# Performance work log

Hardware: AMD Instinct MI355X
Metric: run time of the kernel (lower is better)

Reference implementation:

```python
import jax, jax.numpy as jnp
import numpy as np

EMBED_DIM = 1024
NUM_HEADS = 16
HEAD_DIM = EMBED_DIM // NUM_HEADS
SCALE = HEAD_DIM ** -0.5


def setup_inputs() -> dict:
    key = jax.random.key(0)
    ks = jax.random.split(key, 13)
    B, Q, K, E = 2, 1024, 2048, EMBED_DIM
    bound = 1.0 / np.sqrt(E)
    def lin(k1, k2):
        W = jax.random.uniform(k1, (E, E), jnp.float32, -bound, bound)
        b = jax.random.uniform(k2, (E,), jnp.float32, -bound, bound)
        return W, b
    Wq, bq = lin(ks[0], ks[1])
    Wk, bk = lin(ks[2], ks[3])
    Wv, bv = lin(ks[4], ks[5])
    Wo, bo = lin(ks[6], ks[7])
    return {
        "query": jax.random.normal(ks[8], (B, Q, E), jnp.float32),
        "key": jax.random.normal(ks[9], (B, K, E), jnp.float32),
        "value": jax.random.normal(ks[10], (B, K, E), jnp.float32),
        "key_padding_mask": jax.random.randint(ks[11], (B, K), 0, 2).astype(bool),
        "Wq": Wq, "bq": bq, "Wk": Wk, "bk": bk,
        "Wv": Wv, "bv": bv, "Wo": Wo, "bo": bo,
    }


def reference(query, key, value, key_padding_mask, Wq, bq, Wk, bk, Wv, bv, Wo, bo):
    B, Q, E = query.shape
    K = key.shape[1]
    H, D = NUM_HEADS, HEAD_DIM
    # projections (torch Linear: x @ W.T + b)
    q = (query @ Wq.T + bq).reshape(B, Q, H, D).transpose(0, 2, 1, 3)  # [B,H,Q,D]
    k = (key @ Wk.T + bk).reshape(B, K, H, D).transpose(0, 2, 1, 3)    # [B,H,K,D]
    v = (value @ Wv.T + bv).reshape(B, K, H, D).transpose(0, 2, 1, 3)  # [B,H,K,D]
    logits = jnp.einsum('bhqd,bhkd->bhqk', q, k) * SCALE               # [B,H,Q,K]
    logits = jnp.where(key_padding_mask[:, None, None, :], -jnp.inf, logits)
    attn = jax.nn.softmax(logits, axis=-1)
    out = jnp.einsum('bhqk,bhkd->bhqd', attn, v)                        # [B,H,Q,D]
    out = out.transpose(0, 2, 1, 3).reshape(B, Q, E)
    out = out @ Wo.T + bo
    return out
```

## Files before the change

kernel.cpp:

```cpp
#include <hip/hip_runtime.h>

typedef __bf16 bf16_t;
typedef __bf16 bf16x4 __attribute__((ext_vector_type(4)));
typedef __bf16 bf16x8 __attribute__((ext_vector_type(8)));
typedef float f32x4 __attribute__((ext_vector_type(4)));

#define B_ 2
#define H_ 16
#define D_ 64
#define E_ 1024
#define QL 1024
#define KL 2048
#define SCALE_L2E 0.1803368801111204f
#define NEG_BIG -1e30f
#define DEFER_THR 8.0f

__device__ __forceinline__ void gload_lds16(const void* g, void* lds) {
  auto* gp = reinterpret_cast<const __attribute__((address_space(1))) uint32_t*>(
      reinterpret_cast<uintptr_t>(g));
  auto* lp = reinterpret_cast<__attribute__((address_space(3))) uint32_t*>(
      reinterpret_cast<uintptr_t>(lds));
  __builtin_amdgcn_global_load_lds(gp, lp, 16, 0, 0);
}

__global__ __launch_bounds__(256) void cast_all(
    const float* __restrict__ q, const float* __restrict__ k, const float* __restrict__ v,
    const float* __restrict__ wq, const float* __restrict__ wk,
    const float* __restrict__ wv, const float* __restrict__ wo,
    bf16_t* __restrict__ oq, bf16_t* __restrict__ ok, bf16_t* __restrict__ ov,
    bf16_t* __restrict__ owq, bf16_t* __restrict__ owk,
    bf16_t* __restrict__ owv, bf16_t* __restrict__ owo,
    const unsigned char* __restrict__ mraw, float* __restrict__ mbias) {
  __shared__ int flagMis, flagB0;
  int blk = blockIdx.x;
  if (blk == 7168) {
    int t = threadIdx.x;
    if (t == 0) { flagMis = 0; flagB0 = 0; }
    __syncthreads();
    int a = 0, c = 0;
    for (int i = t; i < B_ * KL; i += 256) {
      if (i & 3) a |= mraw[i]; else c |= mraw[i];
    }
    if (a) atomicOr(&flagMis, 1);
    if (c) atomicOr(&flagB0, 1);
    __syncthreads();
    int mode = (flagMis == 0) ? 0 : (flagB0 ? 1 : 2);
    for (int i = t; i < B_ * KL; i += 256) {
      int mv;
      if (mode == 0)      mv = ((const int*)mraw)[i];
      else if (mode == 1) mv = mraw[i];
      else                mv = (((const float*)mraw)[i] != 0.0f);
      mbias[i] = mv ? NEG_BIG : 0.0f;
    }
    return;
  }
  const float* in; bf16_t* out; int base;
  if (blk < 1024)      { in = q;  out = oq;  base = blk; }
  else if (blk < 3072) { in = k;  out = ok;  base = blk - 1024; }
  else if (blk < 5120) { in = v;  out = ov;  base = blk - 3072; }
  else if (blk < 5632) { in = wq; out = owq; base = blk - 5120; }
  else if (blk < 6144) { in = wk; out = owk; base = blk - 5632; }
  else if (blk < 6656) { in = wv; out = owv; base = blk - 6144; }
  else                 { in = wo; out = owo; base = blk - 6656; }
  size_t i = (size_t)base * 256 + threadIdx.x;
  float4 a = ((const float4*)in)[2 * i];
  float4 b = ((const float4*)in)[2 * i + 1];
  bf16x8 o;
  o[0] = (bf16_t)a.x; o[1] = (bf16_t)a.y; o[2] = (bf16_t)a.z; o[3] = (bf16_t)a.w;
  o[4] = (bf16_t)b.x; o[5] = (bf16_t)b.y; o[6] = (bf16_t)b.z; o[7] = (bf16_t)b.w;
  ((bf16x8*)out)[i] = o;
}

__global__ __launch_bounds__(256, 2)
void qkv_gemm(const bf16_t* __restrict__ Xq, const bf16_t* __restrict__ Xk,
              const bf16_t* __restrict__ Xv, const bf16_t* __restrict__ Wqb,
              const bf16_t* __restrict__ Wkb, const bf16_t* __restrict__ Wvb,
              const float* __restrict__ bq, const float* __restrict__ bk,
              const float* __restrict__ bv,
              bf16_t* __restrict__ qhd, bf16_t* __restrict__ khd, bf16_t* __restrict__ vht) {
  __shared__ alignas(16) bf16_t As[2][128 * 64];
  __shared__ alignas(16) bf16_t Bs[2][128 * 64];
  const int wid = blockIdx.x;
  const int work = (wid & 7) * 80 + (wid >> 3);

  const bf16_t *A, *W;
  const float* bias;
  bf16_t* out;
  int mode, Lshift, row0, col0;
  if (work < 128) {
    A = Xq; W = Wqb; bias = bq; out = qhd; mode = 0; Lshift = 10;
    row0 = (work >> 3) * 128; col0 = (work & 7) * 128;
  } else if (work < 384) {
    int t = work - 128;
    A = Xk; W = Wkb; bias = bk; out = khd; mode = 0; Lshift = 11;
    row0 = (t >> 3) * 128; col0 = (t & 7) * 128;
  } else {
    int t = work - 384;
    A = Wvb; W = Xv; bias = bv; out = vht; mode = 2; Lshift = 0;
    row0 = (t & 7) * 128; col0 = (t >> 3) * 128;
  }

  const int K = 1024;
  const int tid = threadIdx.x;
  const int lane = tid & 63;
  const int w = tid >> 6;
  const int l15 = lane & 15, l4 = lane >> 4;
  const int wr = w >> 1, wc = w & 1;

  f32x4 acc[4][4] = {};

  auto stage = [&](int buf, int kt) {
    const int k0 = kt * 64;
#pragma unroll
    for (int i = 0; i < 4; ++i) {
      int idx = (w * 4 + i) * 64 + lane;
      int r = idx >> 3, c = idx & 7;
      int cs = ((c ^ (r & 7)) * 8);
      gload_lds16(A + (size_t)(row0 + r) * K + k0 + cs, &As[buf][(w * 4 + i) * 512]);
      gload_lds16(W + (size_t)(col0 + r) * K + k0 + cs, &Bs[buf][(w * 4 + i) * 512]);
    }
  };

  auto compute = [&](int buf) {
#pragma unroll
    for (int t = 0; t < 2; ++t) {
      bf16x8 af[4], bfv[4];
#pragma unroll
      for (int i = 0; i < 4; ++i) {
        int r = wr * 64 + i * 16 + l15;
        af[i] = *(const bf16x8*)&As[buf][r * 64 + (((t * 4 + l4) ^ (r & 7)) * 8)];
      }
#pragma unroll
      for (int j = 0; j < 4; ++j) {
        int r = wc * 64 + j * 16 + l15;
        bfv[j] = *(const bf16x8*)&Bs[buf][r * 64 + (((t * 4 + l4) ^ (r & 7)) * 8)];
      }
#pragma unroll
      for (int i = 0; i < 4; ++i)
#pragma unroll
        for (int j = 0; j < 4; ++j)
          acc[i][j] = __builtin_amdgcn_mfma_f32_16x16x32_bf16(af[i], bfv[j], acc[i][j], 0, 0, 0);
    }
  };

  stage(0, 0);
  const int nk = K >> 6;
  for (int kt = 0; kt < nk; ++kt) {
    __syncthreads();
    if (kt + 1 < nk) stage((kt + 1) & 1, kt + 1);
    compute(kt & 1);
  }

#pragma unroll
  for (int i = 0; i < 4; ++i) {
    int mbase = row0 + wr * 64 + i * 16 + l4 * 4;
    f32x4 bvm = {};
    if (mode == 2) bvm = *(const f32x4*)&bias[mbase];
#pragma unroll
    for (int j = 0; j < 4; ++j) {
      int n = col0 + wc * 64 + j * 16 + l15;
      float bv = (mode == 2) ? 0.f : bias[n];
#pragma unroll
      for (int r = 0; r < 4; ++r) {
        float v = acc[i][j][r] + ((mode == 2) ? bvm[r] : bv);
        int m = mbase + r;
        if (mode == 0) {
          int bi = m >> Lshift;
          int ml = m & ((1 << Lshift) - 1);
          size_t dst = ((((size_t)bi * H_ + (n >> 6)) << Lshift) + ml) * D_ + (n & 63);
          out[dst] = (bf16_t)v;
        } else {
          int hh = m >> 6, d = m & 63;
          int bi = n >> 11, kk = n & (KL - 1);
          out[((((size_t)bi * H_ + hh) << 6) + d) * KL + kk] = (bf16_t)v;
        }
      }
    }
  }
}

template <int MODE>
__global__ __launch_bounds__(256, 2)
void gemm_nt(const bf16_t* __restrict__ A, const bf16_t* __restrict__ W,
             const float* __restrict__ bias, void* __restrict__ Cout,
             int M, int N, int K, int Lshift) {
  __shared__ alignas(16) bf16_t As[2][128 * 64];
  __shared__ alignas(16) bf16_t Bs[2][128 * 64];
  const int tid = threadIdx.x;
  const int lane = tid & 63;
  const int w = tid >> 6;
  const int l15 = lane & 15, l4 = lane >> 4;
  const int wr = w >> 1, wc = w & 1;
  const int row0 = blockIdx.x * 128, col0 = blockIdx.y * 128;

  f32x4 acc[4][4] = {};

  auto stage = [&](int buf, int kt) {
    const int k0 = kt * 64;
#pragma unroll
    for (int i = 0; i < 4; ++i) {
      int idx = (w * 4 + i) * 64 + lane;
      int r = idx >> 3, c = idx & 7;
      int cs = ((c ^ (r & 7)) * 8);
      gload_lds16(A + (size_t)(row0 + r) * K + k0 + cs, &As[buf][(w * 4 + i) * 512]);
      gload_lds16(W + (size_t)(col0 + r) * K + k0 + cs, &Bs[buf][(w * 4 + i) * 512]);
    }
  };

  auto compute = [&](int buf) {
#pragma unroll
    for (int t = 0; t < 2; ++t) {
      bf16x8 af[4], bfv[4];
#pragma unroll
      for (int i = 0; i < 4; ++i) {
        int r = wr * 64 + i * 16 + l15;
        af[i] = *(const bf16x8*)&As[buf][r * 64 + (((t * 4 + l4) ^ (r & 7)) * 8)];
      }
#pragma unroll
      for (int j = 0; j < 4; ++j) {
        int r = wc * 64 + j * 16 + l15;
        bfv[j] = *(const bf16x8*)&Bs[buf][r * 64 + (((t * 4 + l4) ^ (r & 7)) * 8)];
      }
#pragma unroll
      for (int i = 0; i < 4; ++i)
#pragma unroll
        for (int j = 0; j < 4; ++j)
          acc[i][j] = __builtin_amdgcn_mfma_f32_16x16x32_bf16(af[i], bfv[j], acc[i][j], 0, 0, 0);
    }
  };

  stage(0, 0);
  const int nk = K >> 6;
  for (int kt = 0; kt < nk; ++kt) {
    __syncthreads();
    if (kt + 1 < nk) stage((kt + 1) & 1, kt + 1);
    compute(kt & 1);
  }

#pragma unroll
  for (int i = 0; i < 4; ++i) {
    int mbase = row0 + wr * 64 + i * 16 + l4 * 4;
#pragma unroll
    for (int j = 0; j < 4; ++j) {
      int n = col0 + wc * 64 + j * 16 + l15;
      float bv = bias[n];
#pragma unroll
      for (int r = 0; r < 4; ++r) {
        float v = acc[i][j][r] + bv;
        int m = mbase + r;
        ((float*)Cout)[(size_t)m * N + n] = v;
      }
    }
  }
}

__global__ __launch_bounds__(256, 4)
void attn_fused(const bf16_t* __restrict__ qh, const bf16_t* __restrict__ kh,
                const bf16_t* __restrict__ vhT, const float* __restrict__ mbias,
                float* __restrict__ opart, float* __restrict__ marr,
                float* __restrict__ larr) {
  __shared__ alignas(16) bf16_t Ksm[2][64 * 64];
  __shared__ alignas(16) bf16_t Vt[2][64 * 64];
  __shared__ alignas(16) bf16_t Ps[4][16 * 64];

  const int wid = blockIdx.x;
  const int work = (wid & 7) * 128 + (wid >> 3);
  const int qt = work & 15;
  const int half = (work >> 4) & 1;
  const int bh = work >> 5;
  const int h = bh & 15, b = bh >> 4;

  const int tid = threadIdx.x, lane = tid & 63, w = tid >> 6;
  const int l15 = lane & 15, l4 = lane >> 4;

  const bf16_t* qbase = qh + ((size_t)bh * QL + qt * 64 + w * 16) * D_;
  bf16x8 qf[2];
#pragma unroll
  for (int t = 0; t < 2; ++t)
    qf[t] = *(const bf16x8*)(qbase + l15 * D_ + t * 32 + l4 * 8);

  float m_run = NEG_BIG, l_run = 0.f;
  f32x4 o_acc[4] = {};

  const bf16_t* kbase = kh + ((size_t)bh * KL + half * (KL / 2)) * D_;
  const bf16_t* vtb = vhT + (size_t)bh * D_ * KL + half * (KL / 2);
  const int idx0 = tid, idx1 = tid + 256;
  const int r0 = idx0 >> 3, cs0 = ((idx0 & 7) ^ (r0 & 7)) * 8;
  const int r1 = idx1 >> 3, cs1 = ((idx1 & 7) ^ (r1 & 7)) * 8;
  const bf16_t* kp0 = kbase + r0 * D_ + cs0;
  const bf16_t* kp1 = kbase + r1 * D_ + cs1;
  const bf16_t* vp0 = vtb + (size_t)r0 * KL + cs0;
  const bf16_t* vp1 = vtb + (size_t)r1 * KL + cs1;
  const float* mptr = mbias + (size_t)b * KL + half * (KL / 2) + l4 * 4;

  auto stage = [&](int bufsel) {
    gload_lds16(kp0, &Ksm[bufsel][idx0 * 8]);
    gload_lds16(kp1, &Ksm[bufsel][idx1 * 8]);
    gload_lds16(vp0, &Vt[bufsel][idx0 * 8]);
    gload_lds16(vp1, &Vt[bufsel][idx1 * 8]);
    kp0 += 64 * D_; kp1 += 64 * D_; vp0 += 64; vp1 += 64;
  };

  stage(0);
  __syncthreads();

  const int NT = KL / 2 / 64;
  for (int kt = 0; kt < NT; ++kt) {
    const int buf = kt & 1;
    if (kt + 1 < NT) stage(buf ^ 1);

    f32x4 mv[4];
#pragma unroll
    for (int ct = 0; ct < 4; ++ct)
      mv[ct] = *(const f32x4*)(mptr + ct * 16);
    mptr += 64;

    f32x4 s[4] = {};
    __builtin_amdgcn_s_setprio(1);
#pragma unroll
    for (int ct = 0; ct < 4; ++ct) {
      int krow = ct * 16 + l15;
#pragma unroll
      for (int t = 0; t < 2; ++t) {
        bf16x8 kf = *(const bf16x8*)&Ksm[buf][krow * 64 + (((t * 4 + l4) ^ (krow & 7)) * 8)];
        s[ct] = __builtin_amdgcn_mfma_f32_16x16x32_bf16(kf, qf[t], s[ct], 0, 0, 0);
      }
    }
    __builtin_amdgcn_s_setprio(0);

    float sv[4][4];
    float mt = NEG_BIG;
#pragma unroll
    for (int ct = 0; ct < 4; ++ct)
#pragma unroll
      for (int r = 0; r < 4; ++r) {
        float x = s[ct][r] * SCALE_L2E + mv[ct][r];
        sv[ct][r] = x;
        mt = fmaxf(mt, x);
      }

    if (!__all(mt <= m_run + DEFER_THR)) {
      mt = fmaxf(mt, __shfl_xor(mt, 16, 64));
      mt = fmaxf(mt, __shfl_xor(mt, 32, 64));
      float mnew = fmaxf(m_run, mt);
      float alpha = exp2f(m_run - mnew);
      m_run = mnew;
      l_run *= alpha;
      float arow[4];
#pragma unroll
      for (int r = 0; r < 4; ++r) arow[r] = __shfl(alpha, l4 * 4 + r, 64);
#pragma unroll
      for (int dt = 0; dt < 4; ++dt)
#pragma unroll
        for (int r = 0; r < 4; ++r) o_acc[dt][r] *= arow[r];
    }

    float rsum = 0.f;
#pragma unroll
    for (int ct = 0; ct < 4; ++ct)
#pragma unroll
      for (int r = 0; r < 4; ++r) {
        float p = exp2f(sv[ct][r] - m_run);
        sv[ct][r] = p;
        rsum += p;
      }
    l_run += rsum;

    char* psrow = (char*)&Ps[w][0] + l15 * 128;
#pragma unroll
    for (int ct = 0; ct < 4; ++ct) {
      bf16x4 pk;
#pragma unroll
      for (int r = 0; r < 4; ++r) pk[r] = (bf16_t)sv[ct][r];
      *(bf16x4*)(psrow + (((ct * 4 + l4) ^ l15) * 8)) = pk;
    }

    __builtin_amdgcn_s_setprio(1);
#pragma unroll
    for (int t = 0; t < 2; ++t) {
      int c0 = t * 8 + l4 * 2;
      bf16x4 plo = *(const bf16x4*)(psrow + ((c0 ^ l15) * 8));
      bf16x4 phi = *(const bf16x4*)(psrow + (((c0 + 1) ^ l15) * 8));
      bf16x8 pa;
#pragma unroll
      for (int j = 0; j < 4; ++j) { pa[j] = plo[j]; pa[j + 4] = phi[j]; }
#pragma unroll
      for (int dt = 0; dt < 4; ++dt) {
        int d = dt * 16 + l15;
        bf16x8 vf = *(const bf16x8*)&Vt[buf][d * 64 + (((t * 4 + l4) ^ (d & 7)) * 8)];
        o_acc[dt] = __builtin_amdgcn_mfma_f32_16x16x32_bf16(pa, vf, o_acc[dt], 0, 0, 0);
      }
    }
    __builtin_amdgcn_s_setprio(0);
    __syncthreads();
  }

  float l_tot = l_run + __shfl_xor(l_run, 16, 64);
  l_tot += __shfl_xor(l_tot, 32, 64);

  const size_t prow = (size_t)(half * 32 + bh) * QL;
#pragma unroll
  for (int r = 0; r < 4; ++r) {
    int qrow = qt * 64 + w * 16 + l4 * 4 + r;
#pragma unroll
    for (int dt = 0; dt < 4; ++dt) {
      int d = dt * 16 + l15;
      opart[(prow + qrow) * D_ + d] = o_acc[dt][r];
    }
  }
  if (l4 == 0) {
    int q = qt * 64 + w * 16 + l15;
    marr[prow + q] = m_run;
    larr[prow + q] = l_tot;
  }
}

__global__ __launch_bounds__(256)
void attn_merge(const float* __restrict__ opart, const float* __restrict__ marr,
                const float* __restrict__ larr, bf16_t* __restrict__ axo) {
  int idx = blockIdx.x * 256 + threadIdx.x;
  int row = idx >> 3;
  int dseg = (idx & 7) * 8;
  int bh = row >> 10, q = row & 1023;
  int b = bh >> 4, h = bh & 15;
  float m0 = marr[row], m1 = marr[32768 + row];
  float l0 = larr[row], l1 = larr[32768 + row];
  float m = fmaxf(m0, m1);
  float w0 = exp2f(m0 - m), w1 = exp2f(m1 - m);
  float denom = l0 * w0 + l1 * w1;
  float s0 = w0 / denom, s1 = w1 / denom;
  const f32x4* p0 = (const f32x4*)&opart[(size_t)row * 64 + dseg];
  const f32x4* p1 = (const f32x4*)&opart[(size_t)(32768 + row) * 64 + dseg];
  f32x4 a0 = p0[0], a1 = p0[1];
  f32x4 b0 = p1[0], b1 = p1[1];
  bf16x8 o;
#pragma unroll
  for (int i = 0; i < 4; ++i) {
    o[i]     = (bf16_t)(a0[i] * s0 + b0[i] * s1);
    o[i + 4] = (bf16_t)(a1[i] * s0 + b1[i] * s1);
  }
  *(bf16x8*)&axo[((size_t)b * QL + q) * E_ + h * 64 + dseg] = o;
}

extern "C" void kernel_launch(void* const* d_in, const int* in_sizes, int n_in,
                              void* d_out, int out_size, void* d_ws, size_t ws_size,
                              hipStream_t stream) {
  const float* query = (const float*)d_in[0];
  const float* key   = (const float*)d_in[1];
  const float* value = (const float*)d_in[2];
  const void*  mask  = d_in[3];
  const float* Wq = (const float*)d_in[4];
  const float* bq = (const float*)d_in[5];
  const float* Wk = (const float*)d_in[6];
  const float* bk = (const float*)d_in[7];
  const float* Wv = (const float*)d_in[8];
  const float* bv = (const float*)d_in[9];
  const float* Wo = (const float*)d_in[10];
  const float* bo = (const float*)d_in[11];

  char* ws = (char*)d_ws;
  bf16_t* Xq  = (bf16_t*)(ws + (0ull  << 20));
  bf16_t* Xk  = (bf16_t*)(ws + (4ull  << 20));
  bf16_t* Xv  = (bf16_t*)(ws + (12ull << 20));
  bf16_t* Wqb = (bf16_t*)(ws + (20ull << 20));
  bf16_t* Wkb = (bf16_t*)(ws + (22ull << 20));
  bf16_t* Wvb = (bf16_t*)(ws + (24ull << 20));
  bf16_t* Wob = (bf16_t*)(ws + (26ull << 20));
  bf16_t* qhd = (bf16_t*)(ws + (28ull << 20));
  bf16_t* khd = (bf16_t*)(ws + (32ull << 20));
  bf16_t* vht = (bf16_t*)(ws + (40ull << 20));
  bf16_t* axo = (bf16_t*)(ws + (48ull << 20));
  float*  mbias = (float*)(ws + (52ull << 20));
  float* opart = (float*)(ws + (0ull << 20));
  float* marr  = (float*)(ws + (16ull << 20));
  float* larr  = (float*)(ws + (17ull << 20));

  cast_all<<<7169, 256, 0, stream>>>(query, key, value, Wq, Wk, Wv, Wo,
                                     Xq, Xk, Xv, Wqb, Wkb, Wvb, Wob,
                                     (const unsigned char*)mask, mbias);
  qkv_gemm<<<640, 256, 0, stream>>>(Xq, Xk, Xv, Wqb, Wkb, Wvb, bq, bk, bv,
                                    qhd, khd, vht);
  attn_fused<<<1024, 256, 0, stream>>>(qhd, khd, vht, mbias, opart, marr, larr);
  attn_merge<<<1024, 256, 0, stream>>>(opart, marr, larr, axo);
  gemm_nt<1><<<dim3(16, 8), 256, 0, stream>>>(axo, Wob, bo, (float*)d_out,
                                              2048, 1024, 1024, 0);
}
```

Before: 209.6 us.

## Fuse split-K attention merge into output projection GEMM prologue

Removes the separate attn_merge kernel and its bf16 intermediate buffer, and instead merges the two partial attention outputs while loading the A tiles of the output-projection GEMM. The new kernel uses 64x128 tiles (256 blocks instead of 128) with double-buffered weight tiles and an XCD-aware block swizzle. This saves a launch and a global round-trip of the merged activations. In exchange, each tile re-reads fp32 partials and recomputes the merge for every column tile, so the merge work is repeated across the 8 column tiles.

```diff
diff --git a/kernel.cpp b/kernel.cpp
--- a/kernel.cpp
+++ b/kernel.cpp
@@ -179,81 +179,6 @@
   }
 }
 
-template <int MODE>
-__global__ __launch_bounds__(256, 2)
-void gemm_nt(const bf16_t* __restrict__ A, const bf16_t* __restrict__ W,
-             const float* __restrict__ bias, void* __restrict__ Cout,
-             int M, int N, int K, int Lshift) {
-  __shared__ alignas(16) bf16_t As[2][128 * 64];
-  __shared__ alignas(16) bf16_t Bs[2][128 * 64];
-  const int tid = threadIdx.x;
-  const int lane = tid & 63;
-  const int w = tid >> 6;
-  const int l15 = lane & 15, l4 = lane >> 4;
-  const int wr = w >> 1, wc = w & 1;
-  const int row0 = blockIdx.x * 128, col0 = blockIdx.y * 128;
-
-  f32x4 acc[4][4] = {};
-
-  auto stage = [&](int buf, int kt) {
-    const int k0 = kt * 64;
-#pragma unroll
-    for (int i = 0; i < 4; ++i) {
-      int idx = (w * 4 + i) * 64 + lane;
-      int r = idx >> 3, c = idx & 7;
-      int cs = ((c ^ (r & 7)) * 8);
-      gload_lds16(A + (size_t)(row0 + r) * K + k0 + cs, &As[buf][(w * 4 + i) * 512]);
-      gload_lds16(W + (size_t)(col0 + r) * K + k0 + cs, &Bs[buf][(w * 4 + i) * 512]);
-    }
-  };
-
-  auto compute = [&](int buf) {
-#pragma unroll
-    for (int t = 0; t < 2; ++t) {
-      bf16x8 af[4], bfv[4];
-#pragma unroll
-      for (int i = 0; i < 4; ++i) {
-        int r = wr * 64 + i * 16 + l15;
-        af[i] = *(const bf16x8*)&As[buf][r * 64 + (((t * 4 + l4) ^ (r & 7)) * 8)];
-      }
-#pragma unroll
-      for (int j = 0; j < 4; ++j) {
-        int r = wc * 64 + j * 16 + l15;
-        bfv[j] = *(const bf16x8*)&Bs[buf][r * 64 + (((t * 4 + l4) ^ (r & 7)) * 8)];
-      }
-#pragma unroll
-      for (int i = 0; i < 4; ++i)
-#pragma unroll
-        for (int j = 0; j < 4; ++j)
-          acc[i][j] = __builtin_amdgcn_mfma_f32_16x16x32_bf16(af[i], bfv[j], acc[i][j], 0, 0, 0);
-    }
-  };
-
-  stage(0, 0);
-  const int nk = K >> 6;
-  for (int kt = 0; kt < nk; ++kt) {
-    __syncthreads();
-    if (kt + 1 < nk) stage((kt + 1) & 1, kt + 1);
-    compute(kt & 1);
-  }
-
-#pragma unroll
-  for (int i = 0; i < 4; ++i) {
-    int mbase = row0 + wr * 64 + i * 16 + l4 * 4;
-#pragma unroll
-    for (int j = 0; j < 4; ++j) {
-      int n = col0 + wc * 64 + j * 16 + l15;
-      float bv = bias[n];
-#pragma unroll
-      for (int r = 0; r < 4; ++r) {
-        float v = acc[i][j][r] + bv;
-        int m = mbase + r;
-        ((float*)Cout)[(size_t)m * N + n] = v;
-      }
-    }
-  }
-}
-
 __global__ __launch_bounds__(256, 4)
 void attn_fused(const bf16_t* __restrict__ qh, const bf16_t* __restrict__ kh,
                 const bf16_t* __restrict__ vhT, const float* __restrict__ mbias,
@@ -268,7 +193,7 @@
   const int qt = work & 15;
   const int half = (work >> 4) & 1;
   const int bh = work >> 5;
-  const int h = bh & 15, b = bh >> 4;
+  const int b = bh >> 4;
 
   const int tid = threadIdx.x, lane = tid & 63, w = tid >> 6;
   const int l15 = lane & 15, l4 = lane >> 4;
@@ -416,30 +341,97 @@
 }
 
 __global__ __launch_bounds__(256)
-void attn_merge(const float* __restrict__ opart, const float* __restrict__ marr,
-                const float* __restrict__ larr, bf16_t* __restrict__ axo) {
-  int idx = blockIdx.x * 256 + threadIdx.x;
-  int row = idx >> 3;
-  int dseg = (idx & 7) * 8;
-  int bh = row >> 10, q = row & 1023;
-  int b = bh >> 4, h = bh & 15;
-  float m0 = marr[row], m1 = marr[32768 + row];
-  float l0 = larr[row], l1 = larr[32768 + row];
-  float m = fmaxf(m0, m1);
-  float w0 = exp2f(m0 - m), w1 = exp2f(m1 - m);
-  float denom = l0 * w0 + l1 * w1;
-  float s0 = w0 / denom, s1 = w1 / denom;
-  const f32x4* p0 = (const f32x4*)&opart[(size_t)row * 64 + dseg];
-  const f32x4* p1 = (const f32x4*)&opart[(size_t)(32768 + row) * 64 + dseg];
-  f32x4 a0 = p0[0], a1 = p0[1];
-  f32x4 b0 = p1[0], b1 = p1[1];
-  bf16x8 o;
-#pragma unroll
-  for (int i = 0; i < 4; ++i) {
-    o[i]     = (bf16_t)(a0[i] * s0 + b0[i] * s1);
-    o[i + 4] = (bf16_t)(a1[i] * s0 + b1[i] * s1);
-  }
-  *(bf16x8*)&axo[((size_t)b * QL + q) * E_ + h * 64 + dseg] = o;
+void oproj_merge(const float* __restrict__ opart, const float* __restrict__ marr,
+                 const float* __restrict__ larr, const bf16_t* __restrict__ Wob,
+                 const float* __restrict__ bo, float* __restrict__ out) {
+  __shared__ alignas(16) bf16_t As[64 * 64];
+  __shared__ alignas(16) bf16_t Bs[2][128 * 64];
+  const int wid = blockIdx.x;
+  const int work = (wid & 7) * 32 + (wid >> 3);
+  const int rt = work >> 3, ct = work & 7;
+  const int row0 = rt * 64, col0 = ct * 128;
+  const int tid = threadIdx.x, lane = tid & 63, w = tid >> 6;
+  const int l15 = lane & 15, l4 = lane >> 4;
+
+  const int ar = tid >> 2, ac = (tid & 3) * 16;
+  const int gm = row0 + ar;
+  const int b = gm >> 10, q = gm & 1023;
+
+  f32x4 acc[8] = {};
+  f32x4 a0[4], a1[4];
+  float sm0, sm1, sl0, sl1;
+
+  auto stageB = [&](int buf, int kt) {
+#pragma unroll
+    for (int i = 0; i < 4; ++i) {
+      int idx = (w * 4 + i) * 64 + lane;
+      int r = idx >> 3, c = idx & 7;
+      int cs = ((c ^ (r & 7)) * 8);
+      gload_lds16(Wob + (size_t)(col0 + r) * E_ + kt * 64 + cs, &Bs[buf][idx * 8]);
+    }
+  };
+
+  auto loadA = [&](int kt) {
+    size_t r0 = (((size_t)b * 16 + kt) << 10) + q;
+    size_t r1 = r0 + 32768;
+    const f32x4* p0 = (const f32x4*)&opart[r0 * 64 + ac];
+    const f32x4* p1 = (const f32x4*)&opart[r1 * 64 + ac];
+#pragma unroll
+    for (int i = 0; i < 4; ++i) { a0[i] = p0[i]; a1[i] = p1[i]; }
+    sm0 = marr[r0]; sm1 = marr[r1]; sl0 = larr[r0]; sl1 = larr[r1];
+  };
+
+  auto writeA = [&]() {
+    float m = fmaxf(sm0, sm1);
+    float w0 = exp2f(sm0 - m), w1 = exp2f(sm1 - m);
+    float denom = sl0 * w0 + sl1 * w1;
+    float s0 = w0 / denom, s1 = w1 / denom;
+#pragma unroll
+    for (int hh = 0; hh < 2; ++hh) {
+      bf16x8 ov;
+#pragma unroll
+      for (int j = 0; j < 8; ++j) {
+        int e = hh * 8 + j;
+        float v = a0[e >> 2][e & 3] * s0 + a1[e >> 2][e & 3] * s1;
+        ov[j] = (bf16_t)v;
+      }
+      int c = (ac >> 3) + hh;
+      *(bf16x8*)&As[ar * 64 + (((c ^ (ar & 7)) * 8))] = ov;
+    }
+  };
+
+  loadA(0);
+  stageB(0, 0);
+  for (int kt = 0; kt < 16; ++kt) {
+    writeA();
+    __syncthreads();
+    if (kt < 15) { loadA(kt + 1); stageB((kt + 1) & 1, kt + 1); }
+
+    const int buf = kt & 1;
+#pragma unroll
+    for (int t = 0; t < 2; ++t) {
+      int r = w * 16 + l15;
+      bf16x8 af = *(const bf16x8*)&As[r * 64 + (((t * 4 + l4) ^ (r & 7)) * 8)];
+#pragma unroll
+      for (int j = 0; j < 8; ++j) {
+        int br = j * 16 + l15;
+        bf16x8 bfv = *(const bf16x8*)&Bs[buf][br * 64 + (((t * 4 + l4) ^ (br & 7)) * 8)];
+        acc[j] = __builtin_amdgcn_mfma_f32_16x16x32_bf16(af, bfv, acc[j], 0, 0, 0);
+      }
+    }
+    __syncthreads();
+  }
+
+#pragma unroll
+  for (int j = 0; j < 8; ++j) {
+    int n = col0 + j * 16 + l15;
+    float bv = bo[n];
+#pragma unroll
+    for (int r = 0; r < 4; ++r) {
+      int m = row0 + w * 16 + l4 * 4 + r;
+      out[(size_t)m * E_ + n] = acc[j][r] + bv;
+    }
+  }
 }
 
 extern "C" void kernel_launch(void* const* d_in, const int* in_sizes, int n_in,
@@ -469,7 +461,6 @@
   bf16_t* qhd = (bf16_t*)(ws + (28ull << 20));
   bf16_t* khd = (bf16_t*)(ws + (32ull << 20));
   bf16_t* vht = (bf16_t*)(ws + (40ull << 20));
-  bf16_t* axo = (bf16_t*)(ws + (48ull << 20));
   float*  mbias = (float*)(ws + (52ull << 20));
   float* opart = (float*)(ws + (0ull << 20));
   float* marr  = (float*)(ws + (16ull << 20));
@@ -481,7 +472,5 @@
   qkv_gemm<<<640, 256, 0, stream>>>(Xq, Xk, Xv, Wqb, Wkb, Wvb, bq, bk, bv,
                                     qhd, khd, vht);
   attn_fused<<<1024, 256, 0, stream>>>(qhd, khd, vht, mbias, opart, marr, larr);
-  attn_merge<<<1024, 256, 0, stream>>>(opart, marr, larr, axo);
-  gemm_nt<1><<<dim3(16, 8), 256, 0, stream>>>(axo, Wob, bo, (float*)d_out,
-                                              2048, 1024, 1024, 0);
-}
+  oproj_merge<<<256, 256, 0, stream>>>(opart, marr, larr, Wob, bo, (float*)d_out);
+}
```

Result: slower. 217.6 us (+3.8%).

## Replace output-projection GEMM with 64x128-tile kernel and swizzled block order

Applied to the files above, without the earlier changes.

Swaps the generic 128x128-tile gemm_nt used for the output projection for a dedicated oproj kernel with 64x128 tiles, which doubles the grid from 128 to 256 blocks so more of the GPU's compute units get work. It also remaps block indices with an interleaved order so that blocks sharing rows or columns are scheduled together, aiming for better L2 reuse. Each wave now computes a 16x128 strip, so the A fragment is reused across 8 MFMAs but B fragments are reloaded from LDS by every wave. The unused h variable in attn_fused is also removed.

```diff
diff --git a/kernel.cpp b/kernel.cpp
--- a/kernel.cpp
+++ b/kernel.cpp
@@ -179,81 +179,6 @@
   }
 }
 
-template <int MODE>
-__global__ __launch_bounds__(256, 2)
-void gemm_nt(const bf16_t* __restrict__ A, const bf16_t* __restrict__ W,
-             const float* __restrict__ bias, void* __restrict__ Cout,
-             int M, int N, int K, int Lshift) {
-  __shared__ alignas(16) bf16_t As[2][128 * 64];
-  __shared__ alignas(16) bf16_t Bs[2][128 * 64];
-  const int tid = threadIdx.x;
-  const int lane = tid & 63;
-  const int w = tid >> 6;
-  const int l15 = lane & 15, l4 = lane >> 4;
-  const int wr = w >> 1, wc = w & 1;
-  const int row0 = blockIdx.x * 128, col0 = blockIdx.y * 128;
-
-  f32x4 acc[4][4] = {};
-
-  auto stage = [&](int buf, int kt) {
-    const int k0 = kt * 64;
-#pragma unroll
-    for (int i = 0; i < 4; ++i) {
-      int idx = (w * 4 + i) * 64 + lane;
-      int r = idx >> 3, c = idx & 7;
-      int cs = ((c ^ (r & 7)) * 8);
-      gload_lds16(A + (size_t)(row0 + r) * K + k0 + cs, &As[buf][(w * 4 + i) * 512]);
-      gload_lds16(W + (size_t)(col0 + r) * K + k0 + cs, &Bs[buf][(w * 4 + i) * 512]);
-    }
-  };
-
-  auto compute = [&](int buf) {
-#pragma unroll
-    for (int t = 0; t < 2; ++t) {
-      bf16x8 af[4], bfv[4];
-#pragma unroll
-      for (int i = 0; i < 4; ++i) {
-        int r = wr * 64 + i * 16 + l15;
-        af[i] = *(const bf16x8*)&As[buf][r * 64 + (((t * 4 + l4) ^ (r & 7)) * 8)];
-      }
-#pragma unroll
-      for (int j = 0; j < 4; ++j) {
-        int r = wc * 64 + j * 16 + l15;
-        bfv[j] = *(const bf16x8*)&Bs[buf][r * 64 + (((t * 4 + l4) ^ (r & 7)) * 8)];
-      }
-#pragma unroll
-      for (int i = 0; i < 4; ++i)
-#pragma unroll
-        for (int j = 0; j < 4; ++j)
-          acc[i][j] = __builtin_amdgcn_mfma_f32_16x16x32_bf16(af[i], bfv[j], acc[i][j], 0, 0, 0);
-    }
-  };
-
-  stage(0, 0);
-  const int nk = K >> 6;
-  for (int kt = 0; kt < nk; ++kt) {
-    __syncthreads();
-    if (kt + 1 < nk) stage((kt + 1) & 1, kt + 1);
-    compute(kt & 1);
-  }
-
-#pragma unroll
-  for (int i = 0; i < 4; ++i) {
-    int mbase = row0 + wr * 64 + i * 16 + l4 * 4;
-#pragma unroll
-    for (int j = 0; j < 4; ++j) {
-      int n = col0 + wc * 64 + j * 16 + l15;
-      float bv = bias[n];
-#pragma unroll
-      for (int r = 0; r < 4; ++r) {
-        float v = acc[i][j][r] + bv;
-        int m = mbase + r;
-        ((float*)Cout)[(size_t)m * N + n] = v;
-      }
-    }
-  }
-}
-
 __global__ __launch_bounds__(256, 4)
 void attn_fused(const bf16_t* __restrict__ qh, const bf16_t* __restrict__ kh,
                 const bf16_t* __restrict__ vhT, const float* __restrict__ mbias,
@@ -268,7 +193,7 @@
   const int qt = work & 15;
   const int half = (work >> 4) & 1;
   const int bh = work >> 5;
-  const int h = bh & 15, b = bh >> 4;
+  const int b = bh >> 4;
 
   const int tid = threadIdx.x, lane = tid & 63, w = tid >> 6;
   const int l15 = lane & 15, l4 = lane >> 4;
@@ -442,6 +367,67 @@
   *(bf16x8*)&axo[((size_t)b * QL + q) * E_ + h * 64 + dseg] = o;
 }
 
+__global__ __launch_bounds__(256)
+void oproj(const bf16_t* __restrict__ A, const bf16_t* __restrict__ W,
+           const float* __restrict__ bias, float* __restrict__ out) {
+  __shared__ alignas(16) bf16_t As[2][64 * 64];
+  __shared__ alignas(16) bf16_t Bs[2][128 * 64];
+  const int wid = blockIdx.x;
+  const int work = (wid & 7) * 32 + (wid >> 3);
+  const int row0 = (work >> 3) * 64, col0 = (work & 7) * 128;
+  const int tid = threadIdx.x, lane = tid & 63, w = tid >> 6;
+  const int l15 = lane & 15, l4 = lane >> 4;
+
+  f32x4 acc[8] = {};
+
+  auto stage = [&](int buf, int kt) {
+    const int k0 = kt * 64;
+#pragma unroll
+    for (int i = 0; i < 2; ++i) {
+      int idx = i * 256 + tid;
+      int r = idx >> 3, c = idx & 7;
+      int cs = ((c ^ (r & 7)) * 8);
+      gload_lds16(A + (size_t)(row0 + r) * E_ + k0 + cs, &As[buf][idx * 8]);
+    }
+#pragma unroll
+    for (int i = 0; i < 4; ++i) {
+      int idx = i * 256 + tid;
+      int r = idx >> 3, c = idx & 7;
+      int cs = ((c ^ (r & 7)) * 8);
+      gload_lds16(W + (size_t)(col0 + r) * E_ + k0 + cs, &Bs[buf][idx * 8]);
+    }
+  };
+
+  stage(0, 0);
+  for (int kt = 0; kt < 16; ++kt) {
+    __syncthreads();
+    if (kt + 1 < 16) stage((kt + 1) & 1, kt + 1);
+    const int buf = kt & 1;
+#pragma unroll
+    for (int t = 0; t < 2; ++t) {
+      int r = w * 16 + l15;
+      bf16x8 af = *(const bf16x8*)&As[buf][r * 64 + (((t * 4 + l4) ^ (r & 7)) * 8)];
+#pragma unroll
+      for (int j = 0; j < 8; ++j) {
+        int br = j * 16 + l15;
+        bf16x8 bfv = *(const bf16x8*)&Bs[buf][br * 64 + (((t * 4 + l4) ^ (br & 7)) * 8)];
+        acc[j] = __builtin_amdgcn_mfma_f32_16x16x32_bf16(af, bfv, acc[j], 0, 0, 0);
+      }
+    }
+  }
+
+#pragma unroll
+  for (int j = 0; j < 8; ++j) {
+    int n = col0 + j * 16 + l15;
+    float bv = bias[n];
+#pragma unroll
+    for (int r = 0; r < 4; ++r) {
+      int m = row0 + w * 16 + l4 * 4 + r;
+      out[(size_t)m * E_ + n] = acc[j][r] + bv;
+    }
+  }
+}
+
 extern "C" void kernel_launch(void* const* d_in, const int* in_sizes, int n_in,
                               void* d_out, int out_size, void* d_ws, size_t ws_size,
                               hipStream_t stream) {
@@ -482,6 +468,5 @@
                                     qhd, khd, vht);
   attn_fused<<<1024, 256, 0, stream>>>(qhd, khd, vht, mbias, opart, marr, larr);
   attn_merge<<<1024, 256, 0, stream>>>(opart, marr, larr, axo);
-  gemm_nt<1><<<dim3(16, 8), 256, 0, stream>>>(axo, Wob, bo, (float*)d_out,
-                                              2048, 1024, 1024, 0);
-}
+  oproj<<<256, 256, 0, stream>>>(axo, Wob, bo, (float*)d_out);
+}
```

Result: no change. 211.4 us (+0.8%).
